# Kernel tuning notes

Hardware: AMD Instinct MI355X
Metric: run time of the kernel (lower is better)

Reference implementation:

```python
import jax, jax.numpy as jnp
import numpy as np

# D2Q9 lattice velocities (standard ordering: rest, axis, diagonal)
E = np.array([[0,0],[1,0],[0,1],[-1,0],[0,-1],[1,1],[-1,1],[-1,-1],[1,-1]], dtype=np.int64)

# Gram-Schmidt moment matrix, row order matches the layer's eq stack:
# [rho, jx, jy, e, eps, qx, qy, pxx, pxy]
_M_np = np.array([
    [ 1,  1,  1,  1,  1,  1,  1,  1,  1],  # rho
    [ 0,  1,  0, -1,  0,  1, -1, -1,  1],  # jx
    [ 0,  0,  1,  0, -1,  1,  1, -1, -1],  # jy
    [-4, -1, -1, -1, -1,  2,  2,  2,  2],  # e
    [ 4, -2, -2, -2, -2,  1,  1,  1,  1],  # eps
    [ 0, -2,  0,  2,  0,  1, -1, -1,  1],  # qx
    [ 0,  0, -2,  0,  2,  1,  1, -1, -1],  # qy
    [ 0,  1, -1,  1, -1,  0,  0,  0,  0],  # pxx
    [ 0,  0,  0,  0,  0,  1, -1,  1, -1],  # pxy
], dtype=np.float64)
_Minv_np = np.linalg.inv(_M_np)

TAU = 0.6
GX, GY = 0.0, -1e-4
ITERATIONS = 4
NX, NY = 1024, 1024


def _stream(f):
    # periodic streaming: shift each population along its lattice velocity
    return jnp.stack(
        [jnp.roll(f[..., i], (int(E[i, 0]), int(E[i, 1])), axis=(0, 1)) for i in range(9)],
        axis=-1,
    )


def setup_inputs() -> dict:
    key = jax.random.key(0)
    kf, kw = jax.random.split(key)
    f = jax.random.uniform(kf, (NX, NY, 9), dtype=jnp.float32)
    w = jax.random.normal(kw, (7,), dtype=jnp.float32)
    return {"f": f, "w": w}


def reference(f, w):
    M = jnp.asarray(_M_np, dtype=f.dtype)
    Minv = jnp.asarray(_Minv_np, dtype=f.dtype)
    ex = jnp.asarray(E[:, 0], dtype=f.dtype)
    ey = jnp.asarray(E[:, 1], dtype=f.dtype)
    inv_tau = jnp.asarray(1.0 / TAU, dtype=f.dtype)

    for _ in range(ITERATIONS):
        # handle_boundaries: periodic (no solid nodes) -> no-op
        f = _stream(f)
        # macroscopic fields
        rho = jnp.sum(f, axis=-1)                      # [X,Y]
        vx = jnp.einsum("xyq,q->xy", f, ex) / rho
        vy = jnp.einsum("xyq,q->xy", f, ey) / rho
        # equilibrium moments with learned coefficients (gravity forcing via tau shift)
        ux = vx + TAU * GX * rho
        uy = vy + TAU * GY * rho
        jx = rho * ux
        jy = rho * uy
        j2 = jx * jx + jy * jy
        e_m = w[0] * rho + w[1] * j2
        eps = w[2] * rho - w[3] * j2
        qx = w[4] * jx
        qy = w[4] * jy
        pxx = w[5] * (jx * jx - jy * jy)
        pxy = w[6] * jx * jy
        meq = jnp.stack([rho, jx, jy, e_m, eps, qx, qy, pxx, pxy], axis=2)
        # collision in moment space, single relaxation rate 1/tau
        m = jnp.einsum("xyq,pq->xyp", f, M)
        m = m - inv_tau * (m - meq)
        f = jnp.einsum("xyp,qp->xyq", m, Minv)
    return f
```

## Files before the change

kernel.cpp:

```cpp
#include <hip/hip_runtime.h>


#define NXD 1024
#define NYD 1024
#define NCELL (NXD * NYD)

constexpr float INV_TAU = (float)(1.0 / 0.6);
constexpr float TGY     = (float)(0.6 * -1e-4);

template <bool SRC_AOS, bool DST_AOS>
__global__ __launch_bounds__(256) void lbm_step(const float* __restrict__ src,
                                                float* __restrict__ dst,
                                                const float* __restrict__ wp) {
    const int cell = blockIdx.x * 256 + threadIdx.x;
    const int x = cell >> 10;
    const int y = cell & (NYD - 1);
    const int xm = (x + NXD - 1) & (NXD - 1);
    const int xp = (x + 1) & (NXD - 1);
    const int ym = (y + NYD - 1) & (NYD - 1);
    const int yp = (y + 1) & (NYD - 1);

    const float w0 = wp[0], w1 = wp[1], w2 = wp[2], w3 = wp[3];
    const float w4 = wp[4], w5 = wp[5], w6 = wp[6];

    float f0, f1, f2, f3, f4, f5, f6, f7, f8;
    if (SRC_AOS) {
        f0 = src[(x  * NYD + y ) * 9 + 0];
        f1 = src[(xm * NYD + y ) * 9 + 1];
        f2 = src[(x  * NYD + ym) * 9 + 2];
        f3 = src[(xp * NYD + y ) * 9 + 3];
        f4 = src[(x  * NYD + yp) * 9 + 4];
        f5 = src[(xm * NYD + ym) * 9 + 5];
        f6 = src[(xp * NYD + ym) * 9 + 6];
        f7 = src[(xp * NYD + yp) * 9 + 7];
        f8 = src[(xm * NYD + yp) * 9 + 8];
    } else {
        f0 = src[0 * NCELL + x  * NYD + y ];
        f1 = src[1 * NCELL + xm * NYD + y ];
        f2 = src[2 * NCELL + x  * NYD + ym];
        f3 = src[3 * NCELL + xp * NYD + y ];
        f4 = src[4 * NCELL + x  * NYD + yp];
        f5 = src[5 * NCELL + xm * NYD + ym];
        f6 = src[6 * NCELL + xp * NYD + ym];
        f7 = src[7 * NCELL + xp * NYD + yp];
        f8 = src[8 * NCELL + xm * NYD + yp];
    }

    const float rho = f0 + f1 + f2 + f3 + f4 + f5 + f6 + f7 + f8;
    const float jx0 = f1 - f3 + f5 - f6 - f7 + f8;
    const float jy0 = f2 - f4 + f5 + f6 - f7 - f8;
    const float vx = jx0 / rho;
    const float vy = jy0 / rho;
    const float uy = vy + TGY * rho;
    const float jx = rho * vx;
    const float jy = rho * uy;
    const float j2 = jx * jx + jy * jy;

    const float ax  = f1 + f2 + f3 + f4;
    const float dg  = f5 + f6 + f7 + f8;
    const float m3 = -4.f * f0 - ax + 2.f * dg;
    const float m4 =  4.f * f0 - 2.f * ax + dg;
    const float m5 = -2.f * f1 + 2.f * f3 + f5 - f6 - f7 + f8;
    const float m6 = -2.f * f2 + 2.f * f4 + f5 + f6 - f7 - f8;
    const float m7 = f1 - f2 + f3 - f4;
    const float m8 = f5 - f6 + f7 - f8;

    const float me3 = w0 * rho + w1 * j2;
    const float me4 = w2 * rho - w3 * j2;
    const float me5 = w4 * jx;
    const float me6 = w4 * jy;
    const float me7 = w5 * (jx * jx - jy * jy);
    const float me8 = w6 * (jx * jy);

    const float mp0 = rho;
    const float mp1 = jx0 - INV_TAU * (jx0 - jx);
    const float mp2 = jy0 - INV_TAU * (jy0 - jy);
    const float mp3 = m3  - INV_TAU * (m3 - me3);
    const float mp4 = m4  - INV_TAU * (m4 - me4);
    const float mp5 = m5  - INV_TAU * (m5 - me5);
    const float mp6 = m6  - INV_TAU * (m6 - me6);
    const float mp7 = m7  - INV_TAU * (m7 - me7);
    const float mp8 = m8  - INV_TAU * (m8 - me8);

    const float s0 = mp0 * (1.f / 9.f);
    const float s1 = mp1 * (1.f / 6.f);
    const float s2 = mp2 * (1.f / 6.f);
    const float s3 = mp3 * (1.f / 36.f);
    const float s4 = mp4 * (1.f / 36.f);
    const float s5 = mp5 * (1.f / 12.f);
    const float s6 = mp6 * (1.f / 12.f);
    const float s7 = mp7 * 0.25f;
    const float s8 = mp8 * 0.25f;

    const float h0 = s0 - s3 - 2.f * s4;
    const float g0 = s0 + 2.f * s3 + s4;

    float fn0 = s0 - 4.f * s3 + 4.f * s4;
    float fn1 = h0 + s1 - 2.f * s5 + s7;
    float fn2 = h0 + s2 - 2.f * s6 - s7;
    float fn3 = h0 - s1 + 2.f * s5 + s7;
    float fn4 = h0 - s2 + 2.f * s6 - s7;
    float fn5 = g0 + s1 + s2 + s5 + s6 + s8;
    float fn6 = g0 - s1 + s2 - s5 + s6 - s8;
    float fn7 = g0 - s1 - s2 - s5 - s6 + s8;
    float fn8 = g0 + s1 - s2 + s5 - s6 - s8;

    if (DST_AOS) {
        float* o = dst + (size_t)(x * NYD + y) * 9;
        o[0] = fn0; o[1] = fn1; o[2] = fn2; o[3] = fn3; o[4] = fn4;
        o[5] = fn5; o[6] = fn6; o[7] = fn7; o[8] = fn8;
    } else {
        const int c = x * NYD + y;
        dst[0 * NCELL + c] = fn0;
        dst[1 * NCELL + c] = fn1;
        dst[2 * NCELL + c] = fn2;
        dst[3 * NCELL + c] = fn3;
        dst[4 * NCELL + c] = fn4;
        dst[5 * NCELL + c] = fn5;
        dst[6 * NCELL + c] = fn6;
        dst[7 * NCELL + c] = fn7;
        dst[8 * NCELL + c] = fn8;
    }
}

extern "C" void kernel_launch(void* const* d_in, const int* in_sizes, int n_in,
                              void* d_out, int out_size, void* d_ws, size_t ws_size,
                              hipStream_t stream) {
    const float* f_in = (const float*)d_in[0];
    const float* w    = (const float*)d_in[1];
    float* out = (float*)d_out;
    float* ws0 = (float*)d_ws;
    const size_t bufBytes = (size_t)NCELL * 9 * sizeof(float);

    dim3 grid(NCELL / 256), block(256);

    if (ws_size >= 2 * bufBytes) {
        float* ws1 = ws0 + (size_t)NCELL * 9;
        lbm_step<true,  false><<<grid, block, 0, stream>>>(f_in, ws0, w);
        lbm_step<false, false><<<grid, block, 0, stream>>>(ws0, ws1, w);
        lbm_step<false, false><<<grid, block, 0, stream>>>(ws1, ws0, w);
        lbm_step<false, true ><<<grid, block, 0, stream>>>(ws0, out, w);
    } else if (ws_size >= bufBytes) {
        lbm_step<true,  false><<<grid, block, 0, stream>>>(f_in, ws0, w);
        lbm_step<false, false><<<grid, block, 0, stream>>>(ws0, out, w);
        lbm_step<false, false><<<grid, block, 0, stream>>>(out, ws0, w);
        lbm_step<false, true ><<<grid, block, 0, stream>>>(ws0, out, w);
    } else {
        float* fin_mut = (float*)d_in[0];
        lbm_step<true, true><<<grid, block, 0, stream>>>(f_in, out, w);
        lbm_step<true, true><<<grid, block, 0, stream>>>(out, fin_mut, w);
        lbm_step<true, true><<<grid, block, 0, stream>>>(fin_mut, out, w);
        lbm_step<true, true><<<grid, block, 0, stream>>>(out, fin_mut, w);
        hipMemcpyAsync(d_out, fin_mut, bufBytes, hipMemcpyDeviceToDevice, stream);
    }
}
```

Measured before the change: 136.8 us.

## Stage AoS rows in shared memory and vectorize SoA steps with float4

```diff
diff --git a/kernel.cpp b/kernel.cpp
--- a/kernel.cpp
+++ b/kernel.cpp
@@ -4,48 +4,18 @@
 #define NXD 1024
 #define NYD 1024
 #define NCELL (NXD * NYD)
+#define ROWF (NYD * 9)
 
 constexpr float INV_TAU = (float)(1.0 / 0.6);
 constexpr float TGY     = (float)(0.6 * -1e-4);
 
-template <bool SRC_AOS, bool DST_AOS>
-__global__ __launch_bounds__(256) void lbm_step(const float* __restrict__ src,
-                                                float* __restrict__ dst,
-                                                const float* __restrict__ wp) {
-    const int cell = blockIdx.x * 256 + threadIdx.x;
-    const int x = cell >> 10;
-    const int y = cell & (NYD - 1);
-    const int xm = (x + NXD - 1) & (NXD - 1);
-    const int xp = (x + 1) & (NXD - 1);
-    const int ym = (y + NYD - 1) & (NYD - 1);
-    const int yp = (y + 1) & (NYD - 1);
-
-    const float w0 = wp[0], w1 = wp[1], w2 = wp[2], w3 = wp[3];
-    const float w4 = wp[4], w5 = wp[5], w6 = wp[6];
-
-    float f0, f1, f2, f3, f4, f5, f6, f7, f8;
-    if (SRC_AOS) {
-        f0 = src[(x  * NYD + y ) * 9 + 0];
-        f1 = src[(xm * NYD + y ) * 9 + 1];
-        f2 = src[(x  * NYD + ym) * 9 + 2];
-        f3 = src[(xp * NYD + y ) * 9 + 3];
-        f4 = src[(x  * NYD + yp) * 9 + 4];
-        f5 = src[(xm * NYD + ym) * 9 + 5];
-        f6 = src[(xp * NYD + ym) * 9 + 6];
-        f7 = src[(xp * NYD + yp) * 9 + 7];
-        f8 = src[(xm * NYD + yp) * 9 + 8];
-    } else {
-        f0 = src[0 * NCELL + x  * NYD + y ];
-        f1 = src[1 * NCELL + xm * NYD + y ];
-        f2 = src[2 * NCELL + x  * NYD + ym];
-        f3 = src[3 * NCELL + xp * NYD + y ];
-        f4 = src[4 * NCELL + x  * NYD + yp];
-        f5 = src[5 * NCELL + xm * NYD + ym];
-        f6 = src[6 * NCELL + xp * NYD + ym];
-        f7 = src[7 * NCELL + xp * NYD + yp];
-        f8 = src[8 * NCELL + xm * NYD + yp];
-    }
-
+__device__ __forceinline__ void collide1(
+    float f0, float f1, float f2, float f3, float f4,
+    float f5, float f6, float f7, float f8,
+    float w0, float w1, float w2, float w3, float w4, float w5, float w6,
+    float& o0, float& o1, float& o2, float& o3, float& o4,
+    float& o5, float& o6, float& o7, float& o8)
+{
     const float rho = f0 + f1 + f2 + f3 + f4 + f5 + f6 + f7 + f8;
     const float jx0 = f1 - f3 + f5 - f6 - f7 + f8;
     const float jy0 = f2 - f4 + f5 + f6 - f7 - f8;
@@ -56,8 +26,8 @@
     const float jy = rho * uy;
     const float j2 = jx * jx + jy * jy;
 
-    const float ax  = f1 + f2 + f3 + f4;
-    const float dg  = f5 + f6 + f7 + f8;
+    const float ax = f1 + f2 + f3 + f4;
+    const float dg = f5 + f6 + f7 + f8;
     const float m3 = -4.f * f0 - ax + 2.f * dg;
     const float m4 =  4.f * f0 - 2.f * ax + dg;
     const float m5 = -2.f * f1 + 2.f * f3 + f5 - f6 - f7 + f8;
@@ -72,7 +42,6 @@
     const float me7 = w5 * (jx * jx - jy * jy);
     const float me8 = w6 * (jx * jy);
 
-    const float mp0 = rho;
     const float mp1 = jx0 - INV_TAU * (jx0 - jx);
     const float mp2 = jy0 - INV_TAU * (jy0 - jy);
     const float mp3 = m3  - INV_TAU * (m3 - me3);
@@ -82,7 +51,7 @@
     const float mp7 = m7  - INV_TAU * (m7 - me7);
     const float mp8 = m8  - INV_TAU * (m8 - me8);
 
-    const float s0 = mp0 * (1.f / 9.f);
+    const float s0 = rho * (1.f / 9.f);
     const float s1 = mp1 * (1.f / 6.f);
     const float s2 = mp2 * (1.f / 6.f);
     const float s3 = mp3 * (1.f / 36.f);
@@ -95,32 +64,213 @@
     const float h0 = s0 - s3 - 2.f * s4;
     const float g0 = s0 + 2.f * s3 + s4;
 
-    float fn0 = s0 - 4.f * s3 + 4.f * s4;
-    float fn1 = h0 + s1 - 2.f * s5 + s7;
-    float fn2 = h0 + s2 - 2.f * s6 - s7;
-    float fn3 = h0 - s1 + 2.f * s5 + s7;
-    float fn4 = h0 - s2 + 2.f * s6 - s7;
-    float fn5 = g0 + s1 + s2 + s5 + s6 + s8;
-    float fn6 = g0 - s1 + s2 - s5 + s6 - s8;
-    float fn7 = g0 - s1 - s2 - s5 - s6 + s8;
-    float fn8 = g0 + s1 - s2 + s5 - s6 - s8;
-
-    if (DST_AOS) {
-        float* o = dst + (size_t)(x * NYD + y) * 9;
-        o[0] = fn0; o[1] = fn1; o[2] = fn2; o[3] = fn3; o[4] = fn4;
-        o[5] = fn5; o[6] = fn6; o[7] = fn7; o[8] = fn8;
-    } else {
-        const int c = x * NYD + y;
-        dst[0 * NCELL + c] = fn0;
-        dst[1 * NCELL + c] = fn1;
-        dst[2 * NCELL + c] = fn2;
-        dst[3 * NCELL + c] = fn3;
-        dst[4 * NCELL + c] = fn4;
-        dst[5 * NCELL + c] = fn5;
-        dst[6 * NCELL + c] = fn6;
-        dst[7 * NCELL + c] = fn7;
-        dst[8 * NCELL + c] = fn8;
-    }
+    o0 = s0 - 4.f * s3 + 4.f * s4;
+    o1 = h0 + s1 - 2.f * s5 + s7;
+    o2 = h0 + s2 - 2.f * s6 - s7;
+    o3 = h0 - s1 + 2.f * s5 + s7;
+    o4 = h0 - s2 + 2.f * s6 - s7;
+    o5 = g0 + s1 + s2 + s5 + s6 + s8;
+    o6 = g0 - s1 + s2 - s5 + s6 - s8;
+    o7 = g0 - s1 - s2 - s5 - s6 + s8;
+    o8 = g0 + s1 - s2 + s5 - s6 - s8;
+}
+
+__device__ __forceinline__ void collide4(const float4 (&F)[9], float4 (&O)[9],
+                                         const float (&w)[7]) {
+    #pragma unroll
+    for (int j = 0; j < 4; ++j) {
+        float f[9], o[9];
+        #pragma unroll
+        for (int q = 0; q < 9; ++q)
+            f[q] = ((const float*)&F[q])[j];
+        collide1(f[0], f[1], f[2], f[3], f[4], f[5], f[6], f[7], f[8],
+                 w[0], w[1], w[2], w[3], w[4], w[5], w[6],
+                 o[0], o[1], o[2], o[3], o[4], o[5], o[6], o[7], o[8]);
+        #pragma unroll
+        for (int q = 0; q < 9; ++q)
+            ((float*)&O[q])[j] = o[q];
+    }
+}
+
+__device__ __forceinline__ float4 ld4s(const float* __restrict__ rowp, int yb) {
+    if (yb >= 0 && yb + 3 < NYD) {
+        float4 v;
+        __builtin_memcpy(&v, rowp + yb, sizeof(float4));
+        return v;
+    }
+    float4 v;
+    v.x = rowp[(yb + 0) & (NYD - 1)];
+    v.y = rowp[(yb + 1) & (NYD - 1)];
+    v.z = rowp[(yb + 2) & (NYD - 1)];
+    v.w = rowp[(yb + 3) & (NYD - 1)];
+    return v;
+}
+
+__device__ __forceinline__ void pull_loads(const float* __restrict__ src,
+                                           int x, int y0, float4 (&F)[9]) {
+    const int xm = (x - 1) & (NXD - 1), xp = (x + 1) & (NXD - 1);
+    const float* p0 = src + 0 * NCELL + x  * NYD;
+    const float* p1 = src + 1 * NCELL + xm * NYD;
+    const float* p2 = src + 2 * NCELL + x  * NYD;
+    const float* p3 = src + 3 * NCELL + xp * NYD;
+    const float* p4 = src + 4 * NCELL + x  * NYD;
+    const float* p5 = src + 5 * NCELL + xm * NYD;
+    const float* p6 = src + 6 * NCELL + xp * NYD;
+    const float* p7 = src + 7 * NCELL + xp * NYD;
+    const float* p8 = src + 8 * NCELL + xm * NYD;
+    __builtin_memcpy(&F[0], p0 + y0, sizeof(float4));
+    __builtin_memcpy(&F[1], p1 + y0, sizeof(float4));
+    __builtin_memcpy(&F[3], p3 + y0, sizeof(float4));
+    F[2] = ld4s(p2, y0 - 1);
+    F[5] = ld4s(p5, y0 - 1);
+    F[6] = ld4s(p6, y0 - 1);
+    F[4] = ld4s(p4, y0 + 1);
+    F[7] = ld4s(p7, y0 + 1);
+    F[8] = ld4s(p8, y0 + 1);
+}
+
+__device__ __forceinline__ void load_w(const float* __restrict__ wp,
+                                       float (&w)[7]) {
+    #pragma unroll
+    for (int i = 0; i < 7; ++i) w[i] = wp[i];
+}
+
+__global__ __launch_bounds__(256) void k1_sc(const float* __restrict__ src,
+                                             float* __restrict__ dst,
+                                             const float* __restrict__ wp) {
+    __shared__ float L[3][258 * 9];
+    const int b   = blockIdx.x;
+    const int x   = b >> 2;
+    const int y0  = (b & 3) << 8;
+    const int tid = threadIdx.x;
+
+    #pragma unroll
+    for (int r = 0; r < 3; ++r) {
+        const int srow = (x - 1 + r) & (NXD - 1);
+        const float* rb = src + (size_t)srow * ROWF;
+        const int base = y0 * 9 - 9;
+        for (int p = tid; p < 258 * 9; p += 256) {
+            int fr = base + p;
+            if (fr < 0) fr += ROWF;
+            else if (fr >= ROWF) fr -= ROWF;
+            L[r][p] = rb[fr];
+        }
+    }
+    __syncthreads();
+
+    float w[7];
+    load_w(wp, w);
+
+    const int ly = tid;
+    const int y  = y0 + ly;
+    const float f0 = L[1][(ly + 1) * 9 + 0];
+    const float f1 = L[0][(ly + 1) * 9 + 1];
+    const float f2 = L[1][(ly + 0) * 9 + 2];
+    const float f3 = L[2][(ly + 1) * 9 + 3];
+    const float f4 = L[1][(ly + 2) * 9 + 4];
+    const float f5 = L[0][(ly + 0) * 9 + 5];
+    const float f6 = L[2][(ly + 0) * 9 + 6];
+    const float f7 = L[2][(ly + 2) * 9 + 7];
+    const float f8 = L[0][(ly + 2) * 9 + 8];
+
+    float o0,o1,o2,o3,o4,o5,o6,o7,o8;
+    collide1(f0,f1,f2,f3,f4,f5,f6,f7,f8,
+             w[0],w[1],w[2],w[3],w[4],w[5],w[6],
+             o0,o1,o2,o3,o4,o5,o6,o7,o8);
+
+    const int c = x * NYD + y;
+    dst[0 * NCELL + c] = o0;
+    dst[1 * NCELL + c] = o1;
+    dst[2 * NCELL + c] = o2;
+    dst[3 * NCELL + c] = o3;
+    dst[4 * NCELL + c] = o4;
+    dst[5 * NCELL + c] = o5;
+    dst[6 * NCELL + c] = o6;
+    dst[7 * NCELL + c] = o7;
+    dst[8 * NCELL + c] = o8;
+}
+
+__global__ __launch_bounds__(256) void k_sc(const float* __restrict__ src,
+                                            float* __restrict__ dst,
+                                            const float* __restrict__ wp) {
+    const int x  = blockIdx.x;
+    const int y0 = threadIdx.x << 2;
+
+    float4 F[9];
+    pull_loads(src, x, y0, F);
+
+    float w[7];
+    load_w(wp, w);
+
+    float4 O[9];
+    collide4(F, O, w);
+
+    const int c = x * NYD + y0;
+    #pragma unroll
+    for (int q = 0; q < 9; ++q)
+        *(float4*)(dst + q * NCELL + c) = O[q];
+}
+
+__global__ __launch_bounds__(256) void k_sc_aos(const float* __restrict__ src,
+                                                float* __restrict__ dst,
+                                                const float* __restrict__ wp) {
+    __shared__ float4 T[ROWF / 4];
+    const int x   = blockIdx.x;
+    const int tid = threadIdx.x;
+    const int y0  = tid << 2;
+
+    float4 F[9];
+    pull_loads(src, x, y0, F);
+
+    float w[7];
+    load_w(wp, w);
+
+    float4 O[9];
+    collide4(F, O, w);
+
+    float* t = (float*)(T + tid * 9);
+    #pragma unroll
+    for (int j = 0; j < 4; ++j) {
+        #pragma unroll
+        for (int q = 0; q < 9; ++q)
+            t[j * 9 + q] = ((const float*)&O[q])[j];
+    }
+    __syncthreads();
+
+    float4* dv = (float4*)(dst + (size_t)x * ROWF);
+    #pragma unroll
+    for (int it = 0; it < 9; ++it)
+        dv[tid + it * 256] = T[tid + it * 256];
+}
+
+__global__ __launch_bounds__(256) void lbm_step_aos(const float* __restrict__ src,
+                                                    float* __restrict__ dst,
+                                                    const float* __restrict__ wp) {
+    const int cell = blockIdx.x * 256 + threadIdx.x;
+    const int x = cell >> 10;
+    const int y = cell & (NYD - 1);
+    const int xm = (x + NXD - 1) & (NXD - 1);
+    const int xp = (x + 1) & (NXD - 1);
+    const int ym = (y + NYD - 1) & (NYD - 1);
+    const int yp = (y + 1) & (NYD - 1);
+
+    const float f0 = src[(x  * NYD + y ) * 9 + 0];
+    const float f1 = src[(xm * NYD + y ) * 9 + 1];
+    const float f2 = src[(x  * NYD + ym) * 9 + 2];
+    const float f3 = src[(xp * NYD + y ) * 9 + 3];
+    const float f4 = src[(x  * NYD + yp) * 9 + 4];
+    const float f5 = src[(xm * NYD + ym) * 9 + 5];
+    const float f6 = src[(xp * NYD + ym) * 9 + 6];
+    const float f7 = src[(xp * NYD + yp) * 9 + 7];
+    const float f8 = src[(xm * NYD + yp) * 9 + 8];
+
+    float o0,o1,o2,o3,o4,o5,o6,o7,o8;
+    collide1(f0,f1,f2,f3,f4,f5,f6,f7,f8,
+             wp[0],wp[1],wp[2],wp[3],wp[4],wp[5],wp[6],
+             o0,o1,o2,o3,o4,o5,o6,o7,o8);
+
+    float* o = dst + (size_t)(x * NYD + y) * 9;
+    o[0]=o0; o[1]=o1; o[2]=o2; o[3]=o3; o[4]=o4; o[5]=o5; o[6]=o6; o[7]=o7; o[8]=o8;
 }
 
 extern "C" void kernel_launch(void* const* d_in, const int* in_sizes, int n_in,
@@ -129,28 +279,21 @@
     const float* f_in = (const float*)d_in[0];
     const float* w    = (const float*)d_in[1];
     float* out = (float*)d_out;
-    float* ws0 = (float*)d_ws;
+    float* A   = (float*)d_ws;
     const size_t bufBytes = (size_t)NCELL * 9 * sizeof(float);
 
-    dim3 grid(NCELL / 256), block(256);
-
     if (ws_size >= 2 * bufBytes) {
-        float* ws1 = ws0 + (size_t)NCELL * 9;
-        lbm_step<true,  false><<<grid, block, 0, stream>>>(f_in, ws0, w);
-        lbm_step<false, false><<<grid, block, 0, stream>>>(ws0, ws1, w);
-        lbm_step<false, false><<<grid, block, 0, stream>>>(ws1, ws0, w);
-        lbm_step<false, true ><<<grid, block, 0, stream>>>(ws0, out, w);
-    } else if (ws_size >= bufBytes) {
-        lbm_step<true,  false><<<grid, block, 0, stream>>>(f_in, ws0, w);
-        lbm_step<false, false><<<grid, block, 0, stream>>>(ws0, out, w);
-        lbm_step<false, false><<<grid, block, 0, stream>>>(out, ws0, w);
-        lbm_step<false, true ><<<grid, block, 0, stream>>>(ws0, out, w);
+        float* B = A + (size_t)NCELL * 9;
+        k1_sc   <<<4096, 256, 0, stream>>>(f_in, A, w);
+        k_sc    <<<1024, 256, 0, stream>>>(A, B, w);
+        k_sc    <<<1024, 256, 0, stream>>>(B, A, w);
+        k_sc_aos<<<1024, 256, 0, stream>>>(A, out, w);
     } else {
         float* fin_mut = (float*)d_in[0];
-        lbm_step<true, true><<<grid, block, 0, stream>>>(f_in, out, w);
-        lbm_step<true, true><<<grid, block, 0, stream>>>(out, fin_mut, w);
-        lbm_step<true, true><<<grid, block, 0, stream>>>(fin_mut, out, w);
-        lbm_step<true, true><<<grid, block, 0, stream>>>(out, fin_mut, w);
+        lbm_step_aos<<<4096, 256, 0, stream>>>(f_in, out, w);
+        lbm_step_aos<<<4096, 256, 0, stream>>>(out, fin_mut, w);
+        lbm_step_aos<<<4096, 256, 0, stream>>>(fin_mut, out, w);
+        lbm_step_aos<<<4096, 256, 0, stream>>>(out, fin_mut, w);
         hipMemcpyAsync(d_out, fin_mut, bufBytes, hipMemcpyDeviceToDevice, stream);
     }
 }
```

New measurement: 164.0 us. 1.2x slower.
